# Optimization experiments

Measured on AMD Instinct MI355X. Metric: run time of the kernel, lower is better.

Reference implementation:

```python
import jax, jax.numpy as jnp
import numpy as np

N, E = 50000, 800000
IN_F, OUT_F, EMB, KER = 64, 64, 3, 4


def setup_inputs() -> dict:
    key = jax.random.key(0)
    ks = jax.random.split(key, 6)
    x = jax.random.normal(ks[0], (N, IN_F), dtype=jnp.float32)
    edge_idx = jax.random.randint(ks[1], (2, E), 0, N, dtype=jnp.int64)
    spec_domain = jax.random.normal(ks[2], (N, EMB), dtype=jnp.float32)
    weight = 0.1 * jax.random.normal(ks[3], (IN_F, OUT_F, KER), dtype=jnp.float32)
    bias_p = 0.1 * jax.random.normal(ks[4], (OUT_F,), dtype=jnp.float32)
    mu = 0.005 * jax.random.normal(ks[5], (EMB, KER), dtype=jnp.float32)
    sig = jnp.ones((1, KER), dtype=jnp.float32)  # repo default 60140 underflows exp with random embeddings
    return {"x": x, "edge_idx": edge_idx, "spec_domain": spec_domain,
            "weight": weight, "bias_p": bias_p, "mu": mu, "sig": sig}


def reference(x, edge_idx, spec_domain, weight, bias_p, mu, sig):
    n = x.shape[0]
    row, col = edge_idx[0], edge_idx[1]
    # support for all kernels at once: [N, out, K]
    support = jnp.einsum('ni,iok->nok', x, weight)
    # per-edge Gaussian kernel values: [E, K]
    diff = spec_domain[row] - spec_domain[col]               # [E, emb]
    dm = diff[:, :, None] - mu[None, :, :]                   # [E, emb, K]
    qq = -0.5 * jnp.sum(dm * dm, axis=1)                     # [E, K]
    value = jnp.exp(sig[0][None, :] * qq)                    # [E, K]
    # sparse mm: out[row] += value * support[col], per kernel
    msgs = value[:, None, :] * support[col]                  # [E, out, K]
    out = jax.ops.segment_sum(msgs, row, num_segments=n)     # [N, out, K]
    return out.sum(axis=2) + bias_p
```

## Files before the change

### kernel.cpp

```cpp
#include <hip/hip_runtime.h>
#include <hip/hip_fp16.h>

#define FIN 64
#define CAP 48
#define BINSH 8
#define NBINMAX 256
#define PCAP 5120
#define TILE_B 4096

__global__ __launch_bounds__(256) void p1_kernel(const float* __restrict__ x,
                                                 const float* __restrict__ weight,
                                                 __half* __restrict__ sup,
                                                 const int* __restrict__ eidx,
                                                 int* __restrict__ gcur,
                                                 int* __restrict__ part,
                                                 int n, int e_total, int sblocks) {
    const int t = threadIdx.x;
    __shared__ float wlds[64 * 256];
    __shared__ int hist[NBINMAX], lbase[NBINMAX], gbase[NBINMAX];
    __shared__ int wsum[4];

    {
        const float4* __restrict__ w4 = (const float4*)weight;
        float4* __restrict__ s4 = (float4*)wlds;
        #pragma unroll
        for (int j = 0; j < 16; ++j) s4[t + j * 256] = w4[t + j * 256];
    }
    __syncthreads();

    {
        const int lane = t & 63;
        const int wid  = t >> 6;
        const int r0 = __builtin_amdgcn_readfirstlane(blockIdx.x * 32 + wid * 8);
        if (r0 + 7 < n) {
            const float* __restrict__ xr = x + (size_t)r0 * 64;

            float4 acc[8];
            #pragma unroll
            for (int r = 0; r < 8; ++r) acc[r] = make_float4(0.f, 0.f, 0.f, 0.f);

            #pragma unroll 4
            for (int ic = 0; ic < 16; ++ic) {
                float4 w0 = *(const float4*)&wlds[(ic * 4 + 0) * 256 + lane * 4];
                float4 w1 = *(const float4*)&wlds[(ic * 4 + 1) * 256 + lane * 4];
                float4 w2 = *(const float4*)&wlds[(ic * 4 + 2) * 256 + lane * 4];
                float4 w3 = *(const float4*)&wlds[(ic * 4 + 3) * 256 + lane * 4];
                #pragma unroll
                for (int r = 0; r < 8; ++r) {
                    float4 xv = *(const float4*)&xr[r * 64 + ic * 4];
                    acc[r].x += xv.x * w0.x + xv.y * w1.x + xv.z * w2.x + xv.w * w3.x;
                    acc[r].y += xv.x * w0.y + xv.y * w1.y + xv.z * w2.y + xv.w * w3.y;
                    acc[r].z += xv.x * w0.z + xv.y * w1.z + xv.z * w2.z + xv.w * w3.z;
                    acc[r].w += xv.x * w0.w + xv.y * w1.w + xv.z * w2.w + xv.w * w3.w;
                }
            }

            #pragma unroll
            for (int r = 0; r < 8; ++r) {
                union { __half2 h[2]; uint2 u; } p;
                p.h[0] = __floats2half2_rn(acc[r].x, acc[r].y);
                p.h[1] = __floats2half2_rn(acc[r].z, acc[r].w);
                *(uint2*)&sup[(size_t)(r0 + r) * 256 + lane * 4] = p.u;
            }
        }
    }

    if (blockIdx.x < sblocks) {
        int nz = 0;
        #pragma unroll
        for (int j = 1; j < 16; j += 2) nz |= eidx[j];
        const int is64 = (nz == 0);

        hist[t] = 0;
        __syncthreads();

        const int base = blockIdx.x * TILE_B;
        int nv = e_total - base;
        if (nv > TILE_B) nv = TILE_B;
        if (nv < 0) nv = 0;

        int pay[16], bn[16], lp[16];
        #pragma unroll
        for (int i = 0; i < 8; ++i) {
            const int pl = t + 256 * i;
            const int pg = (base >> 1) + pl;
            int r0 = 0, c0 = 0, r1 = 0, c1 = 0, v0 = 0, v1 = 0;
            if (2 * pl < nv) {
                if (is64) {
                    int4 rr = ((const int4*)eidx)[pg];
                    int4 cc = ((const int4*)(eidx + 2 * (size_t)e_total))[pg];
                    r0 = rr.x; c0 = cc.x; v0 = 1;
                    if (2 * pl + 1 < nv) { r1 = rr.z; c1 = cc.z; v1 = 1; }
                } else {
                    int2 rr = ((const int2*)eidx)[pg];
                    int2 cc = ((const int2*)(eidx + (size_t)e_total))[pg];
                    r0 = rr.x; c0 = cc.x; v0 = 1;
                    if (2 * pl + 1 < nv) { r1 = rr.y; c1 = cc.y; v1 = 1; }
                }
            }
            pay[2 * i]     = (c0 << 8) | (r0 & 255);
            bn[2 * i]      = v0 ? (r0 >> BINSH) : -1;
            pay[2 * i + 1] = (c1 << 8) | (r1 & 255);
            bn[2 * i + 1]  = v1 ? (r1 >> BINSH) : -1;
        }
        #pragma unroll
        for (int i = 0; i < 16; ++i) {
            lp[i] = (bn[i] >= 0) ? atomicAdd(&hist[bn[i]], 1) : 0;
        }
        __syncthreads();

        {
            const int lane = t & 63;
            const int w = t >> 6;
            int h = hist[t];
            int s = h;
            #pragma unroll
            for (int off = 1; off < 64; off <<= 1) {
                int u = __shfl_up(s, off, 64);
                if (lane >= off) s += u;
            }
            if (lane == 63) wsum[w] = s;
            __syncthreads();
            if (t == 0) {
                int a = 0;
                #pragma unroll
                for (int q = 0; q < 4; ++q) { int u = wsum[q]; wsum[q] = a; a += u; }
            }
            __syncthreads();
            lbase[t] = s - h + wsum[w];
            gbase[t] = (h > 0) ? atomicAdd(&gcur[t], h) : 0;
        }
        __syncthreads();

        #pragma unroll
        for (int i = 0; i < 16; ++i) {
            if (bn[i] >= 0) {
                int dst = gbase[bn[i]] + lp[i];
                if (dst < PCAP) part[bn[i] * PCAP + dst] = pay[i];
            }
        }
    }
}

__global__ __launch_bounds__(1024) void p2_kernel(const int* __restrict__ gcur,
                                                  const int* __restrict__ part,
                                                  const float* __restrict__ spec,
                                                  const float* __restrict__ mu,
                                                  const float* __restrict__ sig,
                                                  int* __restrict__ cnt,
                                                  int* __restrict__ scol,
                                                  uint2* __restrict__ sval, int n) {
    __shared__ int cl[256];
    const int t = threadIdx.x;
    const int b = blockIdx.x;
    const int row0 = b << BINSH;
    if (t < 256) cl[t] = 0;
    __syncthreads();

    float m0[4], m1[4], m2[4], sg[4];
    #pragma unroll
    for (int k = 0; k < 4; ++k) {
        m0[k] = mu[k]; m1[k] = mu[4 + k]; m2[k] = mu[8 + k]; sg[k] = sig[k];
    }

    int nloc = gcur[b];
    if (nloc > PCAP) nloc = PCAP;
    const int* __restrict__ mypart = part + b * PCAP;

    for (int i = t; i < nloc; i += 1024) {
        int e = mypart[i];
        int rl = e & 255;
        int col = ((unsigned)e) >> 8;
        int row = row0 + rl;

        float d0 = spec[row * 3 + 0] - spec[col * 3 + 0];
        float d1 = spec[row * 3 + 1] - spec[col * 3 + 1];
        float d2 = spec[row * 3 + 2] - spec[col * 3 + 2];
        float v[4];
        #pragma unroll
        for (int k = 0; k < 4; ++k) {
            float a = d0 - m0[k], bb = d1 - m1[k], c = d2 - m2[k];
            v[k] = __expf(sg[k] * (-0.5f * (a * a + bb * bb + c * c)));
        }
        union { __half2 h; unsigned u; } p01, p23;
        p01.h = __floats2half2_rn(v[0], v[1]);
        p23.h = __floats2half2_rn(v[2], v[3]);

        int pos = atomicAdd(&cl[rl], 1);
        if (pos < CAP) {
            scol[(size_t)row * CAP + pos] = col;
            sval[(size_t)row * CAP + pos] = make_uint2(p01.u, p23.u);
        }
    }
    __syncthreads();

    int row = row0 + t;
    if (t < 256 && row < n) cnt[row] = (cl[t] > CAP) ? CAP : cl[t];
}

__device__ __forceinline__ float dot_supv(uint2 p, uint2 pv) {
    float2 f0 = __half22float2(__builtin_bit_cast(__half2, p.x));
    float2 f1 = __half22float2(__builtin_bit_cast(__half2, p.y));
    float2 a0 = __half22float2(__builtin_bit_cast(__half2, pv.x));
    float2 a1 = __half22float2(__builtin_bit_cast(__half2, pv.y));
    return f0.x * a0.x + f0.y * a0.y + f1.x * a1.x + f1.y * a1.y;
}

__global__ __launch_bounds__(256, 6) void row_kernel(const int* __restrict__ cnt,
                                                     const int* __restrict__ scol,
                                                     const uint2* __restrict__ sval,
                                                     const __half* __restrict__ sup,
                                                     const float* __restrict__ bias,
                                                     float* __restrict__ out, int n) {
    const int lane = threadIdx.x & 63;
    const int wl = threadIdx.x >> 6;
    const int wv = __builtin_amdgcn_readfirstlane(blockIdx.x * 4 + wl);
    const int NW = gridDim.x * 4;
    const float bias_l = bias[lane];
    const unsigned un = (unsigned)n;

    for (int r = wv; r < n; r += NW) {
        int ec = cnt[r];
        if (ec > CAP) ec = CAP;
        const size_t base = (size_t)r * CAP;
        float acc = bias_l;

        for (int j = 0; j < ec; j += 16) {
            int c[16]; uint2 w[16];
            #pragma unroll
            for (int i = 0; i < 16; ++i) {
                int idx = j + i;
                int cc = scol[base + idx];
                uint2 ww = sval[base + idx];
                bool valid = idx < ec;
                c[i] = ((unsigned)cc < un) ? cc : 0;
                w[i] = valid ? ww : make_uint2(0u, 0u);
            }
            uint2 p[16];
            #pragma unroll
            for (int i = 0; i < 16; ++i)
                p[i] = *(const uint2*)(sup + ((size_t)c[i] * 256 + lane * 4));
            #pragma unroll
            for (int i = 0; i < 16; ++i)
                acc += dot_supv(p[i], w[i]);
        }
        out[(size_t)r * 64 + lane] = acc;
    }
}

extern "C" void kernel_launch(void* const* d_in, const int* in_sizes, int n_in,
                              void* d_out, int out_size, void* d_ws, size_t ws_size,
                              hipStream_t stream) {
    const float* x      = (const float*)d_in[0];
    const int*   eidx   = (const int*)d_in[1];
    const float* spec   = (const float*)d_in[2];
    const float* weight = (const float*)d_in[3];
    const float* bias   = (const float*)d_in[4];
    const float* mu     = (const float*)d_in[5];
    const float* sig    = (const float*)d_in[6];
    float* out = (float*)d_out;

    const int N = in_sizes[0] / FIN;
    const int E = in_sizes[1] / 2;
    const int NB32 = (N + 31) / 32;
    const int SBLK = (E + TILE_B - 1) / TILE_B;
    const int NBIN = (N + (1 << BINSH) - 1) >> BINSH;

    char* w = (char*)d_ws;
    size_t off = 0;
    int* gcur = (int*)(w + off);            off += NBINMAX * 4;
    __half* sup = (__half*)(w + off);       off += (size_t)N * 256 * sizeof(__half);
    off = (off + 255) & ~(size_t)255;
    int* cnt = (int*)(w + off);             off += (size_t)N * 4;
    off = (off + 255) & ~(size_t)255;
    int* scol = (int*)(w + off);            off += (size_t)N * CAP * 4;
    off = (off + 255) & ~(size_t)255;
    uint2* sval = (uint2*)(w + off);        off += (size_t)N * CAP * 8;
    off = (off + 255) & ~(size_t)255;
    int* part = (int*)(w + off);            off += (size_t)NBIN * PCAP * 4;

    hipMemsetAsync(gcur, 0, NBINMAX * 4, stream);
    p1_kernel<<<NB32, 256, 0, stream>>>(x, weight, sup, eidx, gcur, part, N, E, SBLK);
    p2_kernel<<<NBIN, 1024, 0, stream>>>(gcur, part, spec, mu, sig, cnt, scol, sval, N);
    row_kernel<<<1536, 256, 0, stream>>>(cnt, scol, sval, sup, bias, out, N);
}
```

Baseline: 120.0 us.

## Compute support projection with bf16 MFMA instead of scalar FP32 FMAs

Replaces the scalar FP32 x·W product in p1 with bf16 16x16x32 MFMA instructions. Each block stages its 32 rows of x into LDS as bf16, and each wave reads its weight fragment directly from global memory and converts it to bf16, so the 64 KB weight copy into LDS goes away. It also handles partial row tiles instead of skipping them. The aim is to cut ALU and LDS time in the projection phase, at the cost of bf16 precision on the inputs and scattered 2-byte stores of the half-precision output.

After: 105.0 us (median of 2 runs). 12.5% less time.

```diff
diff --git a/kernel.cpp b/kernel.cpp
--- a/kernel.cpp
+++ b/kernel.cpp
@@ -7,6 +7,17 @@
 #define NBINMAX 256
 #define PCAP 5120
 #define TILE_B 4096
+
+typedef __attribute__((ext_vector_type(8))) short short8v;
+typedef __attribute__((ext_vector_type(4))) float f32x4v;
+
+__device__ __forceinline__ unsigned pk_bf16(float a, float b) {
+    unsigned ua = __builtin_bit_cast(unsigned, a);
+    unsigned ub = __builtin_bit_cast(unsigned, b);
+    ua = (ua + 0x7FFFu + ((ua >> 16) & 1u)) >> 16;
+    ub = (ub + 0x7FFFu + ((ub >> 16) & 1u)) >> 16;
+    return ua | (ub << 16);
+}
 
 __global__ __launch_bounds__(256) void p1_kernel(const float* __restrict__ x,
                                                  const float* __restrict__ weight,
@@ -16,51 +27,80 @@
                                                  int* __restrict__ part,
                                                  int n, int e_total, int sblocks) {
     const int t = threadIdx.x;
-    __shared__ float wlds[64 * 256];
+    __shared__ unsigned short xb[32][72];
     __shared__ int hist[NBINMAX], lbase[NBINMAX], gbase[NBINMAX];
     __shared__ int wsum[4];
 
-    {
-        const float4* __restrict__ w4 = (const float4*)weight;
-        float4* __restrict__ s4 = (float4*)wlds;
-        #pragma unroll
-        for (int j = 0; j < 16; ++j) s4[t + j * 256] = w4[t + j * 256];
-    }
-    __syncthreads();
-
-    {
+    const int rowbase = blockIdx.x * 32;
+    if (rowbase < n) {
+        {
+            int nrows = n - rowbase; if (nrows > 32) nrows = 32;
+            int nf2 = nrows * 32;
+            const float2* __restrict__ x2 = (const float2*)(x + (size_t)rowbase * 64);
+            #pragma unroll
+            for (int j = 0; j < 4; ++j) {
+                int idx = t + j * 256;
+                if (idx < nf2) {
+                    float2 v = x2[idx];
+                    int r = idx >> 5, c2 = idx & 31;
+                    *(unsigned*)&xb[r][c2 * 2] = pk_bf16(v.x, v.y);
+                }
+            }
+        }
+        __syncthreads();
+
         const int lane = t & 63;
-        const int wid  = t >> 6;
-        const int r0 = __builtin_amdgcn_readfirstlane(blockIdx.x * 32 + wid * 8);
-        if (r0 + 7 < n) {
-            const float* __restrict__ xr = x + (size_t)r0 * 64;
-
-            float4 acc[8];
-            #pragma unroll
-            for (int r = 0; r < 8; ++r) acc[r] = make_float4(0.f, 0.f, 0.f, 0.f);
-
-            #pragma unroll 4
-            for (int ic = 0; ic < 16; ++ic) {
-                float4 w0 = *(const float4*)&wlds[(ic * 4 + 0) * 256 + lane * 4];
-                float4 w1 = *(const float4*)&wlds[(ic * 4 + 1) * 256 + lane * 4];
-                float4 w2 = *(const float4*)&wlds[(ic * 4 + 2) * 256 + lane * 4];
-                float4 w3 = *(const float4*)&wlds[(ic * 4 + 3) * 256 + lane * 4];
+        const int w4 = t >> 6;
+        const int lm = lane & 15, lg = lane >> 4;
+
+        short8v a[2][2];
+        #pragma unroll
+        for (int mt = 0; mt < 2; ++mt)
+            #pragma unroll
+            for (int kb = 0; kb < 2; ++kb)
+                a[mt][kb] = *(const short8v*)&xb[mt * 16 + lm][kb * 32 + lg * 8];
+
+        f32x4v acc[2][4];
+        #pragma unroll
+        for (int mt = 0; mt < 2; ++mt)
+            #pragma unroll
+            for (int nt = 0; nt < 4; ++nt)
+                acc[mt][nt] = (f32x4v){0.f, 0.f, 0.f, 0.f};
+
+        #pragma unroll
+        for (int nt = 0; nt < 4; ++nt) {
+            const int col = (w4 * 4 + nt) * 16 + lm;
+            short8v bfr[2];
+            #pragma unroll
+            for (int kb = 0; kb < 2; ++kb) {
+                short8v bb;
                 #pragma unroll
-                for (int r = 0; r < 8; ++r) {
-                    float4 xv = *(const float4*)&xr[r * 64 + ic * 4];
-                    acc[r].x += xv.x * w0.x + xv.y * w1.x + xv.z * w2.x + xv.w * w3.x;
-                    acc[r].y += xv.x * w0.y + xv.y * w1.y + xv.z * w2.y + xv.w * w3.y;
-                    acc[r].z += xv.x * w0.z + xv.y * w1.z + xv.z * w2.z + xv.w * w3.z;
-                    acc[r].w += xv.x * w0.w + xv.y * w1.w + xv.z * w2.w + xv.w * w3.w;
+                for (int j = 0; j < 8; ++j) {
+                    float wv = weight[(kb * 32 + lg * 8 + j) * 256 + col];
+                    unsigned u = __builtin_bit_cast(unsigned, wv);
+                    bb[j] = (short)((u + 0x7FFFu + ((u >> 16) & 1u)) >> 16);
                 }
-            }
-
-            #pragma unroll
-            for (int r = 0; r < 8; ++r) {
-                union { __half2 h[2]; uint2 u; } p;
-                p.h[0] = __floats2half2_rn(acc[r].x, acc[r].y);
-                p.h[1] = __floats2half2_rn(acc[r].z, acc[r].w);
-                *(uint2*)&sup[(size_t)(r0 + r) * 256 + lane * 4] = p.u;
+                bfr[kb] = bb;
+            }
+            #pragma unroll
+            for (int mt = 0; mt < 2; ++mt) {
+                acc[mt][nt] = __builtin_amdgcn_mfma_f32_16x16x32_bf16(a[mt][0], bfr[0], acc[mt][nt], 0, 0, 0);
+                acc[mt][nt] = __builtin_amdgcn_mfma_f32_16x16x32_bf16(a[mt][1], bfr[1], acc[mt][nt], 0, 0, 0);
+            }
+        }
+
+        #pragma unroll
+        for (int mt = 0; mt < 2; ++mt) {
+            const int row0 = rowbase + mt * 16 + lg * 4;
+            #pragma unroll
+            for (int reg = 0; reg < 4; ++reg) {
+                if (row0 + reg < n) {
+                    #pragma unroll
+                    for (int nt = 0; nt < 4; ++nt) {
+                        int col = (w4 * 4 + nt) * 16 + lm;
+                        sup[(size_t)(row0 + reg) * 256 + col] = __float2half(acc[mt][nt][reg]);
+                    }
+                }
             }
         }
     }
@@ -122,9 +162,9 @@
             if (lane == 63) wsum[w] = s;
             __syncthreads();
             if (t == 0) {
-                int a = 0;
+                int a0 = 0;
                 #pragma unroll
-                for (int q = 0; q < 4; ++q) { int u = wsum[q]; wsum[q] = a; a += u; }
+                for (int q = 0; q < 4; ++q) { int u = wsum[q]; wsum[q] = a0; a0 += u; }
             }
             __syncthreads();
             lbase[t] = s - h + wsum[w];
```
